# Performance work log

Measured on AMD Instinct MI355X. Metric: run time of the kernel, lower is better.

The kernel has to match this reference:

```python
import jax, jax.numpy as jnp
import numpy as np

DT = 1.0 / 60.0  # physics timestep
NUM_BODY = 20

# ---- quaternion helpers (xyzw convention, matching the repo) ----

def quat_from_rotvec(rv):
    # rv: [..., 3] axis-angle -> quaternion [..., 4] (x,y,z,w)
    angle = jnp.linalg.norm(rv, axis=-1, keepdims=True)
    half = 0.5 * angle
    safe = jnp.where(angle < 1e-8, 1.0, angle)
    s = jnp.where(angle < 1e-8, 0.5 - angle * angle / 48.0, jnp.sin(half) / safe)
    return jnp.concatenate([rv * s, jnp.cos(half)], axis=-1)


def flip_quat_by_w(q):
    return jnp.where(q[..., 3:4] < 0, -q, q)


def quat_to_vec6d(q):
    # first two columns of the rotation matrix, row-major flattened -> [..., 6]
    x, y, z, w = q[..., 0], q[..., 1], q[..., 2], q[..., 3]
    r00 = 1 - 2 * (y * y + z * z)
    r10 = 2 * (x * y + z * w)
    r20 = 2 * (x * z - y * w)
    r01 = 2 * (x * y - z * w)
    r11 = 1 - 2 * (x * x + z * z)
    r21 = 2 * (y * z + x * w)
    return jnp.stack([r00, r01, r10, r11, r20, r21], axis=-1)


def quat_apply(q, v):
    # rotate v [..., 3] by quaternion q [..., 4]; broadcasts over leading dims
    xyz, w = q[..., :3], q[..., 3:4]
    t = 2.0 * jnp.cross(xyz, v)
    return v + w * t + jnp.cross(xyz, t)


def quat_multiply(p, q):
    pv, pw = p[..., :3], p[..., 3:4]
    qv, qw = q[..., :3], q[..., 3:4]
    v = pw * qv + qw * pv + jnp.cross(pv, qv)
    w = pw * qw - jnp.sum(pv * qv, axis=-1, keepdims=True)
    return jnp.concatenate([v, w], axis=-1)


def quat_integrate(q, omega, dt):
    # q_{t+1} = normalize(q + 0.5*dt * (omega_quat * q))
    omega_q = jnp.concatenate([omega, jnp.zeros_like(omega[..., :1])], axis=-1)
    dq = quat_multiply(omega_q, q)
    r = q + 0.5 * dt * dq
    return r / jnp.linalg.norm(r, axis=-1, keepdims=True)


def integrate_state(state, delta, dt):
    # state: [B, NB, 13] = pos(3) | rot quat(4) | vel(3) | avel(3)
    B, NB, _ = state.shape
    pos, rot = state[..., 0:3], state[..., 3:7]
    vel, avel = state[..., 7:10], state[..., 10:13]
    root_rot = state[:, 0:1, 3:7]                       # [B, 1, 4]
    d3 = delta.reshape(B, -1, 3)                        # [B, 2*NB, 3]
    true_d = quat_apply(root_rot, d3).reshape(B, NB, 6)
    lin, ang = true_d[..., :3], true_d[..., 3:]
    next_vel = vel + lin
    next_avel = avel + ang
    next_pos = pos + next_vel * dt
    next_rot = quat_integrate(rot, next_avel, dt)
    return jnp.concatenate([next_pos, next_rot, next_vel, next_avel], axis=-1)


def setup_inputs() -> dict:
    key = jax.random.key(0)
    ks = jax.random.split(key, 12)
    B = 32768
    inp = {
        "state": jax.random.normal(ks[0], (B, NUM_BODY, 13), jnp.float32),
        "action": jax.random.normal(ks[1], (B, 57), jnp.float32),
        "n_observation": jax.random.normal(ks[2], (B, 300), jnp.float32),
        "W1": jax.random.normal(ks[3], (414, 512), jnp.float32) * 0.05,
        "b1": jax.random.normal(ks[4], (512,), jnp.float32) * 0.05,
        "W2": jax.random.normal(ks[5], (512, 512), jnp.float32) * 0.05,
        "b2": jax.random.normal(ks[6], (512,), jnp.float32) * 0.05,
        "W3": jax.random.normal(ks[7], (512, 120), jnp.float32) * 0.05,
        "b3": jax.random.normal(ks[8], (120,), jnp.float32) * 0.05,
        "delta_mean": jax.random.normal(ks[9], (120,), jnp.float32) * 0.01,
        "delta_std": jax.random.uniform(ks[10], (120,), jnp.float32) + 0.5,
    }
    return inp


def reference(state, action, n_observation, W1, b1, W2, b2, W3, b3, delta_mean, delta_std):
    B = action.shape[0]
    # action rotvecs -> quats -> 6d representation
    aq = flip_quat_by_w(quat_from_rotvec(action.reshape(-1, 3)))
    a6 = quat_to_vec6d(aq).reshape(B, -1)               # [B, 114]
    x = jnp.concatenate([n_observation, a6], axis=-1)   # [B, 414]
    h = jax.nn.relu(x @ W1 + b1)
    h = jax.nn.relu(h @ W2 + b2)
    n_delta = h @ W3 + b3                                # [B, 120]
    delta = n_delta * delta_std + delta_mean             # unnormalize
    return integrate_state(state, delta, DT)
```

## Files before the change

### kernel.cpp

```cpp
#include <hip/hip_runtime.h>
#include <hip/hip_bf16.h>
#include <math.h>

#define DT (1.0f / 60.0f)

typedef __bf16 bf16x8 __attribute__((ext_vector_type(8)));
typedef float f32x4 __attribute__((ext_vector_type(4)));

#define XSTRIDE 848
#define HSTRIDE 1040

__global__ __launch_bounds__(256) void prep_weights(
    const float* __restrict__ W1, const float* __restrict__ W2,
    const float* __restrict__ W3, __hip_bfloat16* __restrict__ W1p,
    __hip_bfloat16* __restrict__ W2p, __hip_bfloat16* __restrict__ W3p) {
    int idx = blockIdx.x * 256 + threadIdx.x;
    if (idx < 212992) {
        int d = idx;
        int e = d & 7, l = (d >> 3) & 63, t = d >> 9;
        int nt = t & 31, ks = t >> 5;
        int n = nt * 16 + (l & 15);
        int k = ks * 32 + (l >> 4) * 8 + e;
        W1p[d] = __float2bfloat16(k < 414 ? W1[k * 512 + n] : 0.0f);
        return;
    }
    idx -= 212992;
    if (idx < 262144) {
        int d = idx;
        int e = d & 7, l = (d >> 3) & 63, t = d >> 9;
        int nt = t & 31, ks = t >> 5;
        int n = nt * 16 + (l & 15);
        int k = ks * 32 + (l >> 4) * 8 + e;
        W2p[d] = __float2bfloat16(W2[k * 512 + n]);
        return;
    }
    idx -= 262144;
    if (idx < 65536) {
        int d = idx;
        int e = d & 7, l = (d >> 3) & 63, t = d >> 9;
        int nt = t & 7, ks = t >> 3;
        int n = nt * 16 + (l & 15);
        int k = ks * 32 + (l >> 4) * 8 + e;
        W3p[d] = __float2bfloat16(n < 120 ? W3[k * 120 + n] : 0.0f);
    }
}

template <int KSTEPS, int NT, int ASTRIDE>
__device__ __forceinline__ void mlp_layer(const char* Abase, const char* Bbase,
                                          int laneOff, f32x4 (&acc)[4][8]) {
    bf16x8 b0[8], b1[8];
#pragma unroll
    for (int j = 0; j < 8; j++)
        b0[j] = *(const bf16x8*)(Bbase + (j << 10) + laneOff);
#pragma unroll
    for (int ks = 0; ks < KSTEPS; ks++) {
        if (ks + 1 < KSTEPS) {
            if ((ks & 1) == 0) {
#pragma unroll
                for (int j = 0; j < 8; j++)
                    b1[j] = *(const bf16x8*)(Bbase + (((ks + 1) * NT + j) << 10) + laneOff);
            } else {
#pragma unroll
                for (int j = 0; j < 8; j++)
                    b0[j] = *(const bf16x8*)(Bbase + (((ks + 1) * NT + j) << 10) + laneOff);
            }
        }
        bf16x8 af[4];
#pragma unroll
        for (int i = 0; i < 4; i++)
            af[i] = *(const bf16x8*)(Abase + ks * 64 + i * 16 * ASTRIDE);
#pragma unroll
        for (int i = 0; i < 4; i++)
#pragma unroll
            for (int j = 0; j < 8; j++)
                acc[i][j] = __builtin_amdgcn_mfma_f32_16x16x32_bf16(
                    af[i], (ks & 1) ? b1[j] : b0[j], acc[i][j], 0, 0, 0);
    }
}

__device__ __forceinline__ void store_h_relu(const f32x4 (&acc)[4][8],
                                             char* smem, const float* bias,
                                             int wm, int wn, int lrow,
                                             int kgrp) {
#pragma unroll
    for (int j = 0; j < 8; j++) {
        int col = wn * 128 + j * 16 + lrow;
        float bb = bias[col];
#pragma unroll
        for (int i = 0; i < 4; i++) {
            char* p = smem + (wm * 64 + i * 16 + kgrp * 4) * HSTRIDE + col * 2;
#pragma unroll
            for (int r = 0; r < 4; r++) {
                float v = acc[i][j][r] + bb;
                v = v > 0.0f ? v : 0.0f;
                *(__hip_bfloat16*)(p + r * HSTRIDE) = __float2bfloat16(v);
            }
        }
    }
}

__device__ __forceinline__ void quat_apply3(float qx, float qy, float qz,
                                            float qw, float vx, float vy,
                                            float vz, float& ox, float& oy,
                                            float& oz) {
    float tx = 2.0f * (qy * vz - qz * vy);
    float ty = 2.0f * (qz * vx - qx * vz);
    float tz = 2.0f * (qx * vy - qy * vx);
    ox = vx + qw * tx + (qy * tz - qz * ty);
    oy = vy + qw * ty + (qz * tx - qx * tz);
    oz = vz + qw * tz + (qx * ty - qy * tx);
}

__global__ __launch_bounds__(512, 2) void fused_mlp(
    const float* __restrict__ obs, const float* __restrict__ action,
    const __hip_bfloat16* __restrict__ W1p, const float* __restrict__ b1,
    const __hip_bfloat16* __restrict__ W2p, const float* __restrict__ b2,
    const __hip_bfloat16* __restrict__ W3p, const float* __restrict__ b3,
    const float* __restrict__ dstd, const float* __restrict__ dmean,
    const float* __restrict__ state, float* __restrict__ out) {
    alignas(16) __shared__ char smem[128 * HSTRIDE];
    const int tid = threadIdx.x;
    const int blk = blockIdx.x;
    const int lane = tid & 63, w = tid >> 6;
    const int wm = w >> 2, wn = w & 3;
    const int lrow = lane & 15, kgrp = lane >> 4;
    const int laneOff = lane * 16;

    {
        const float4* og = (const float4*)obs + (size_t)blk * 128 * 75;
#pragma unroll
        for (int i = 0; i < 19; i++) {
            int f = tid + i * 512;
            if (f < 9600) {
                int row = f / 75;
                int c4 = f - row * 75;
                float4 v = og[f];
                union { __hip_bfloat16 h[4]; uint2 u; } pk;
                pk.h[0] = __float2bfloat16(v.x);
                pk.h[1] = __float2bfloat16(v.y);
                pk.h[2] = __float2bfloat16(v.z);
                pk.h[3] = __float2bfloat16(v.w);
                *(uint2*)(smem + row * XSTRIDE + c4 * 8) = pk.u;
            }
        }
#pragma unroll
        for (int i = 0; i < 5; i++) {
            int q = tid + i * 512;
            if (q < 2432) {
                int row = q / 19;
                int j = q - row * 19;
                const float* a = action + ((size_t)(blk * 128 + row)) * 57 + j * 3;
                float rx = a[0], ry = a[1], rz = a[2];
                float ang = sqrtf(rx * rx + ry * ry + rz * rz);
                float half = 0.5f * ang;
                float s;
                if (ang < 1e-8f)
                    s = 0.5f - ang * ang * (1.0f / 48.0f);
                else
                    s = sinf(half) / ang;
                float qx = rx * s, qy = ry * s, qz = rz * s, qw = cosf(half);
                union { __hip_bfloat16 h[6]; uint u[3]; } pq;
                pq.h[0] = __float2bfloat16(1.0f - 2.0f * (qy * qy + qz * qz));
                pq.h[1] = __float2bfloat16(2.0f * (qx * qy - qz * qw));
                pq.h[2] = __float2bfloat16(2.0f * (qx * qy + qz * qw));
                pq.h[3] = __float2bfloat16(1.0f - 2.0f * (qx * qx + qz * qz));
                pq.h[4] = __float2bfloat16(2.0f * (qx * qz - qy * qw));
                pq.h[5] = __float2bfloat16(2.0f * (qy * qz + qx * qw));
                char* p = smem + row * XSTRIDE + 600 + j * 12;
                *(uint*)p = pq.u[0];
                *(uint*)(p + 4) = pq.u[1];
                *(uint*)(p + 8) = pq.u[2];
            }
        }
#pragma unroll
        for (int i = 0; i < 2; i++) {
            int id = tid + i * 512;
            if (id < 640) {
                int row = id / 5;
                int p = id - row * 5;
                *(uint*)(smem + row * XSTRIDE + 828 + p * 4) = 0u;
            }
        }
    }
    __syncthreads();

    f32x4 acc[4][8];
    f32x4 zero4 = {0.0f, 0.0f, 0.0f, 0.0f};
#pragma unroll
    for (int i = 0; i < 4; i++)
#pragma unroll
        for (int j = 0; j < 8; j++) acc[i][j] = zero4;

    mlp_layer<13, 32, XSTRIDE>(smem + (wm * 64 + lrow) * XSTRIDE + kgrp * 16,
                               (const char*)W1p + (wn << 13), laneOff, acc);
    __syncthreads();
    store_h_relu(acc, smem, b1, wm, wn, lrow, kgrp);
    __syncthreads();

#pragma unroll
    for (int i = 0; i < 4; i++)
#pragma unroll
        for (int j = 0; j < 8; j++) acc[i][j] = zero4;
    mlp_layer<16, 32, HSTRIDE>(smem + (wm * 64 + lrow) * HSTRIDE + kgrp * 16,
                               (const char*)W2p + (wn << 13), laneOff, acc);
    __syncthreads();
    store_h_relu(acc, smem, b2, wm, wn, lrow, kgrp);
    __syncthreads();

    f32x4 a3[8];
#pragma unroll
    for (int j = 0; j < 8; j++) a3[j] = zero4;
    {
        const char* Ab = smem + (w * 16 + lrow) * HSTRIDE + kgrp * 16;
        const char* Bb = (const char*)W3p;
        bf16x8 c0[8], c1[8];
#pragma unroll
        for (int j = 0; j < 8; j++)
            c0[j] = *(const bf16x8*)(Bb + (j << 10) + laneOff);
#pragma unroll
        for (int ks = 0; ks < 16; ks++) {
            if (ks + 1 < 16) {
                if ((ks & 1) == 0) {
#pragma unroll
                    for (int j = 0; j < 8; j++)
                        c1[j] = *(const bf16x8*)(Bb + (((ks + 1) * 8 + j) << 10) + laneOff);
                } else {
#pragma unroll
                    for (int j = 0; j < 8; j++)
                        c0[j] = *(const bf16x8*)(Bb + (((ks + 1) * 8 + j) << 10) + laneOff);
                }
            }
            bf16x8 a = *(const bf16x8*)(Ab + ks * 64);
#pragma unroll
            for (int j = 0; j < 8; j++)
                a3[j] = __builtin_amdgcn_mfma_f32_16x16x32_bf16(
                    a, (ks & 1) ? c1[j] : c0[j], a3[j], 0, 0, 0);
        }
    }
    __syncthreads();

    float* dl = (float*)smem;
#pragma unroll
    for (int j = 0; j < 8; j++) {
        int col = j * 16 + lrow;
        if (col < 120) {
            float bb = b3[col], sc = dstd[col], mn = dmean[col];
#pragma unroll
            for (int r = 0; r < 4; r++) {
                int row = w * 16 + kgrp * 4 + r;
                dl[row * 120 + col] = (a3[j][r] + bb) * sc + mn;
            }
        }
    }
    __syncthreads();

#pragma unroll
    for (int it = 0; it < 5; it++) {
        int idx = tid + it * 512;
        int lr = idx / 20;
        int body = idx - lr * 20;
        int rowg = blk * 128 + lr;
        const float* sb = state + (size_t)rowg * 260 + body * 13;
        const float* rq = state + (size_t)rowg * 260 + 3;
        float qx = rq[0], qy = rq[1], qz = rq[2], qw = rq[3];
        const float* d = dl + lr * 120 + body * 6;

        float lx, ly, lz, ax, ay, az;
        quat_apply3(qx, qy, qz, qw, d[0], d[1], d[2], lx, ly, lz);
        quat_apply3(qx, qy, qz, qw, d[3], d[4], d[5], ax, ay, az);

        float vx = sb[7] + lx, vy = sb[8] + ly, vz = sb[9] + lz;
        float wx = sb[10] + ax, wy = sb[11] + ay, wz = sb[12] + az;
        float px = sb[0] + vx * DT, py = sb[1] + vy * DT, pz = sb[2] + vz * DT;

        float rx = sb[3], ry = sb[4], rz = sb[5], rw = sb[6];
        float dqx = rw * wx + (wy * rz - wz * ry);
        float dqy = rw * wy + (wz * rx - wx * rz);
        float dqz = rw * wz + (wx * ry - wy * rx);
        float dqw = -(wx * rx + wy * ry + wz * rz);
        float h = 0.5f * DT;
        float nx = rx + h * dqx, ny = ry + h * dqy, nz = rz + h * dqz,
              nw = rw + h * dqw;
        float inv = 1.0f / sqrtf(nx * nx + ny * ny + nz * nz + nw * nw);

        float* o = out + (size_t)rowg * 260 + body * 13;
        o[0] = px;
        o[1] = py;
        o[2] = pz;
        o[3] = nx * inv;
        o[4] = ny * inv;
        o[5] = nz * inv;
        o[6] = nw * inv;
        o[7] = vx;
        o[8] = vy;
        o[9] = vz;
        o[10] = wx;
        o[11] = wy;
        o[12] = wz;
    }
}

extern "C" void kernel_launch(void* const* d_in, const int* in_sizes, int n_in,
                              void* d_out, int out_size, void* d_ws,
                              size_t ws_size, hipStream_t stream) {
    const float* state = (const float*)d_in[0];
    const float* action = (const float*)d_in[1];
    const float* obs = (const float*)d_in[2];
    const float* W1 = (const float*)d_in[3];
    const float* b1 = (const float*)d_in[4];
    const float* W2 = (const float*)d_in[5];
    const float* b2 = (const float*)d_in[6];
    const float* W3 = (const float*)d_in[7];
    const float* b3 = (const float*)d_in[8];
    const float* dmean = (const float*)d_in[9];
    const float* dstd = (const float*)d_in[10];
    float* out = (float*)d_out;
    char* ws = (char*)d_ws;

    const int B = in_sizes[1] / 57;

    __hip_bfloat16* W1p = (__hip_bfloat16*)(ws);
    __hip_bfloat16* W2p = (__hip_bfloat16*)(ws + 425984);
    __hip_bfloat16* W3p = (__hip_bfloat16*)(ws + 950272);

    prep_weights<<<2112, 256, 0, stream>>>(W1, W2, W3, W1p, W2p, W3p);
    fused_mlp<<<B / 128, 512, 0, stream>>>(obs, action, W1p, b1, W2p, b2, W3p,
                                           b3, dstd, dmean, state, out);
}
```

Before: 179.0 us.

## Halve rows per block to 64 with four waves; repartition layer-3 tiles

The fused MLP block now covers 64 batch rows with 256 threads (4 waves split across N) instead of 128 rows with 512 threads. The grid doubles and the shared-memory footprint halves. The layer-3 GEMM is repartitioned so each wave computes a 64x32 output slice over four M-subtiles and two N-subtiles, instead of a 16x128 slice. The K loops are also limited to unroll 2. The aim is more blocks for load balance and occupancy with less LDS per block, at the cost of each block reusing the bf16 weights over half as many rows, which doubles weight traffic from L2.

New measurement: 167.3 us. 6.6% less time.

```diff
diff --git a/kernel.cpp b/kernel.cpp
--- a/kernel.cpp
+++ b/kernel.cpp
@@ -52,7 +52,7 @@
 #pragma unroll
     for (int j = 0; j < 8; j++)
         b0[j] = *(const bf16x8*)(Bbase + (j << 10) + laneOff);
-#pragma unroll
+#pragma unroll 2
     for (int ks = 0; ks < KSTEPS; ks++) {
         if (ks + 1 < KSTEPS) {
             if ((ks & 1) == 0) {
@@ -80,15 +80,14 @@
 
 __device__ __forceinline__ void store_h_relu(const f32x4 (&acc)[4][8],
                                              char* smem, const float* bias,
-                                             int wm, int wn, int lrow,
-                                             int kgrp) {
+                                             int wn, int lrow, int kgrp) {
 #pragma unroll
     for (int j = 0; j < 8; j++) {
         int col = wn * 128 + j * 16 + lrow;
         float bb = bias[col];
 #pragma unroll
         for (int i = 0; i < 4; i++) {
-            char* p = smem + (wm * 64 + i * 16 + kgrp * 4) * HSTRIDE + col * 2;
+            char* p = smem + (i * 16 + kgrp * 4) * HSTRIDE + col * 2;
 #pragma unroll
             for (int r = 0; r < 4; r++) {
                 float v = acc[i][j][r] + bb;
@@ -111,27 +110,26 @@
     oz = vz + qw * tz + (qx * ty - qy * tx);
 }
 
-__global__ __launch_bounds__(512, 2) void fused_mlp(
+__global__ __launch_bounds__(256, 2) void fused_mlp(
     const float* __restrict__ obs, const float* __restrict__ action,
     const __hip_bfloat16* __restrict__ W1p, const float* __restrict__ b1,
     const __hip_bfloat16* __restrict__ W2p, const float* __restrict__ b2,
     const __hip_bfloat16* __restrict__ W3p, const float* __restrict__ b3,
     const float* __restrict__ dstd, const float* __restrict__ dmean,
     const float* __restrict__ state, float* __restrict__ out) {
-    alignas(16) __shared__ char smem[128 * HSTRIDE];
+    alignas(16) __shared__ char smem[64 * HSTRIDE];
     const int tid = threadIdx.x;
     const int blk = blockIdx.x;
-    const int lane = tid & 63, w = tid >> 6;
-    const int wm = w >> 2, wn = w & 3;
+    const int lane = tid & 63, wn = tid >> 6;
     const int lrow = lane & 15, kgrp = lane >> 4;
     const int laneOff = lane * 16;
 
     {
-        const float4* og = (const float4*)obs + (size_t)blk * 128 * 75;
+        const float4* og = (const float4*)obs + (size_t)blk * 64 * 75;
 #pragma unroll
         for (int i = 0; i < 19; i++) {
-            int f = tid + i * 512;
-            if (f < 9600) {
+            int f = tid + i * 256;
+            if (f < 4800) {
                 int row = f / 75;
                 int c4 = f - row * 75;
                 float4 v = og[f];
@@ -145,11 +143,11 @@
         }
 #pragma unroll
         for (int i = 0; i < 5; i++) {
-            int q = tid + i * 512;
-            if (q < 2432) {
+            int q = tid + i * 256;
+            if (q < 1216) {
                 int row = q / 19;
                 int j = q - row * 19;
-                const float* a = action + ((size_t)(blk * 128 + row)) * 57 + j * 3;
+                const float* a = action + ((size_t)(blk * 64 + row)) * 57 + j * 3;
                 float rx = a[0], ry = a[1], rz = a[2];
                 float ang = sqrtf(rx * rx + ry * ry + rz * rz);
                 float half = 0.5f * ang;
@@ -174,8 +172,8 @@
         }
 #pragma unroll
         for (int i = 0; i < 2; i++) {
-            int id = tid + i * 512;
-            if (id < 640) {
+            int id = tid + i * 256;
+            if (id < 320) {
                 int row = id / 5;
                 int p = id - row * 5;
                 *(uint*)(smem + row * XSTRIDE + 828 + p * 4) = 0u;
@@ -191,64 +189,74 @@
 #pragma unroll
         for (int j = 0; j < 8; j++) acc[i][j] = zero4;
 
-    mlp_layer<13, 32, XSTRIDE>(smem + (wm * 64 + lrow) * XSTRIDE + kgrp * 16,
+    mlp_layer<13, 32, XSTRIDE>(smem + lrow * XSTRIDE + kgrp * 16,
                                (const char*)W1p + (wn << 13), laneOff, acc);
     __syncthreads();
-    store_h_relu(acc, smem, b1, wm, wn, lrow, kgrp);
+    store_h_relu(acc, smem, b1, wn, lrow, kgrp);
     __syncthreads();
 
 #pragma unroll
     for (int i = 0; i < 4; i++)
 #pragma unroll
         for (int j = 0; j < 8; j++) acc[i][j] = zero4;
-    mlp_layer<16, 32, HSTRIDE>(smem + (wm * 64 + lrow) * HSTRIDE + kgrp * 16,
+    mlp_layer<16, 32, HSTRIDE>(smem + lrow * HSTRIDE + kgrp * 16,
                                (const char*)W2p + (wn << 13), laneOff, acc);
     __syncthreads();
-    store_h_relu(acc, smem, b2, wm, wn, lrow, kgrp);
-    __syncthreads();
-
-    f32x4 a3[8];
-#pragma unroll
-    for (int j = 0; j < 8; j++) a3[j] = zero4;
+    store_h_relu(acc, smem, b2, wn, lrow, kgrp);
+    __syncthreads();
+
+    f32x4 a3[4][2];
+#pragma unroll
+    for (int i = 0; i < 4; i++)
+#pragma unroll
+        for (int j = 0; j < 2; j++) a3[i][j] = zero4;
     {
-        const char* Ab = smem + (w * 16 + lrow) * HSTRIDE + kgrp * 16;
+        const char* Ab = smem + lrow * HSTRIDE + kgrp * 16;
         const char* Bb = (const char*)W3p;
-        bf16x8 c0[8], c1[8];
-#pragma unroll
-        for (int j = 0; j < 8; j++)
-            c0[j] = *(const bf16x8*)(Bb + (j << 10) + laneOff);
-#pragma unroll
+        bf16x8 c0[2], c1[2];
+#pragma unroll
+        for (int j = 0; j < 2; j++)
+            c0[j] = *(const bf16x8*)(Bb + ((wn * 2 + j) << 10) + laneOff);
+#pragma unroll 2
         for (int ks = 0; ks < 16; ks++) {
             if (ks + 1 < 16) {
                 if ((ks & 1) == 0) {
 #pragma unroll
-                    for (int j = 0; j < 8; j++)
-                        c1[j] = *(const bf16x8*)(Bb + (((ks + 1) * 8 + j) << 10) + laneOff);
+                    for (int j = 0; j < 2; j++)
+                        c1[j] = *(const bf16x8*)(Bb + (((ks + 1) * 8 + wn * 2 + j) << 10) + laneOff);
                 } else {
 #pragma unroll
-                    for (int j = 0; j < 8; j++)
-                        c0[j] = *(const bf16x8*)(Bb + (((ks + 1) * 8 + j) << 10) + laneOff);
+                    for (int j = 0; j < 2; j++)
+                        c0[j] = *(const bf16x8*)(Bb + (((ks + 1) * 8 + wn * 2 + j) << 10) + laneOff);
                 }
             }
-            bf16x8 a = *(const bf16x8*)(Ab + ks * 64);
-#pragma unroll
-            for (int j = 0; j < 8; j++)
-                a3[j] = __builtin_amdgcn_mfma_f32_16x16x32_bf16(
-                    a, (ks & 1) ? c1[j] : c0[j], a3[j], 0, 0, 0);
+            bf16x8 af[4];
+#pragma unroll
+            for (int i = 0; i < 4; i++)
+                af[i] = *(const bf16x8*)(Ab + ks * 64 + i * 16 * HSTRIDE);
+#pragma unroll
+            for (int i = 0; i < 4; i++)
+#pragma unroll
+                for (int j = 0; j < 2; j++)
+                    a3[i][j] = __builtin_amdgcn_mfma_f32_16x16x32_bf16(
+                        af[i], (ks & 1) ? c1[j] : c0[j], a3[i][j], 0, 0, 0);
         }
     }
     __syncthreads();
 
     float* dl = (float*)smem;
 #pragma unroll
-    for (int j = 0; j < 8; j++) {
-        int col = j * 16 + lrow;
+    for (int j = 0; j < 2; j++) {
+        int col = wn * 32 + j * 16 + lrow;
         if (col < 120) {
             float bb = b3[col], sc = dstd[col], mn = dmean[col];
 #pragma unroll
-            for (int r = 0; r < 4; r++) {
-                int row = w * 16 + kgrp * 4 + r;
-                dl[row * 120 + col] = (a3[j][r] + bb) * sc + mn;
+            for (int i = 0; i < 4; i++) {
+#pragma unroll
+                for (int r = 0; r < 4; r++) {
+                    int row = i * 16 + kgrp * 4 + r;
+                    dl[row * 120 + col] = (a3[i][j][r] + bb) * sc + mn;
+                }
             }
         }
     }
@@ -256,10 +264,10 @@
 
 #pragma unroll
     for (int it = 0; it < 5; it++) {
-        int idx = tid + it * 512;
+        int idx = tid + it * 256;
         int lr = idx / 20;
         int body = idx - lr * 20;
-        int rowg = blk * 128 + lr;
+        int rowg = blk * 64 + lr;
         const float* sb = state + (size_t)rowg * 260 + body * 13;
         const float* rq = state + (size_t)rowg * 260 + 3;
         float qx = rq[0], qy = rq[1], qz = rq[2], qw = rq[3];
@@ -324,6 +332,6 @@
     __hip_bfloat16* W3p = (__hip_bfloat16*)(ws + 950272);
 
     prep_weights<<<2112, 256, 0, stream>>>(W1, W2, W3, W1p, W2p, W3p);
-    fused_mlp<<<B / 128, 512, 0, stream>>>(obs, action, W1p, b1, W2p, b2, W3p,
-                                           b3, dstd, dmean, state, out);
-}
+    fused_mlp<<<B / 64, 256, 0, stream>>>(obs, action, W1p, b1, W2p, b2, W3p,
+                                          b3, dstd, dmean, state, out);
+}
```
